# Optimization experiments

Hardware: AMD Instinct MI355X
Metric: run time of the kernel (lower is better)

The kernel has to match this reference:

```python
import jax, jax.numpy as jnp
import numpy as np

NEARZERO = 1e-5
NMUL = 16
NSTEP = 365
NGRID = 10000

# change_param_range: lb + raw * (ub - lb)
HBV_BOUNDS = {'parBETA': (1.0, 6.0), 'parK0': (0.05, 0.9), 'parBETAET': (0.3, 5.0)}
WL_BOUNDS = {'parFC': (50.0, 1000.0), 'parK1': (0.01, 0.5), 'parK2': (0.001, 0.2),
             'parLP': (0.2, 1.0), 'parPERC': (0.0, 10.0), 'parUZL': (0.0, 100.0),
             'parTT': (-2.5, 2.5), 'parCFMAX': (0.5, 10.0), 'parCFR': (0.0, 0.1),
             'parCWH': (0.0, 0.2), 'parC': (0.0, 1.0), 'parTRbound': (0.0, 20.0),
             'parAc': (0.0, 2500.0)}


def setup_inputs() -> dict:
    key = jax.random.key(0)
    kP, kT, kE, kp, kw, ka = jax.random.split(key, 6)
    P = jax.random.uniform(kP, (NSTEP, NGRID)) * 20.0          # precip [mm/day]
    T = jax.random.uniform(kT, (NSTEP, NGRID)) * 30.0 - 5.0    # temp [C]
    PET = jax.random.uniform(kE, (NSTEP, NGRID)) * 6.0         # PET [mm/day]
    x_hydro_model = jnp.stack([P, T, PET], axis=-1)            # [Nstep, Ngrid, 3]
    params_raw = jax.random.uniform(kp, (NSTEP, NGRID, 3, NMUL))
    waterloss_params_raw = jax.random.uniform(kw, (NGRID, 13, NMUL))
    ac_batch = jax.random.uniform(ka, (NGRID,)) * 3000.0       # drainage area proxy
    return {'x_hydro_model': x_hydro_model, 'params_raw': params_raw,
            'waterloss_params_raw': waterloss_params_raw, 'ac_batch': ac_batch}


def _scale_params(params_raw, waterloss_params_raw, static_idx=-1):
    p = {}
    for i, (name, (lb, ub)) in enumerate(HBV_BOUNDS.items()):
        p[name] = lb + params_raw[static_idx, :, i, :] * (ub - lb)       # [Ngrid, nmul]
    for i, (name, (lb, ub)) in enumerate(WL_BOUNDS.items()):
        p[name] = lb + waterloss_params_raw[:, i, :] * (ub - lb)         # [Ngrid, nmul]
    return p


def reference(x_hydro_model, params_raw, waterloss_params_raw, ac_batch):
    p = _scale_params(params_raw, waterloss_params_raw)
    P = x_hydro_model[:, :, 0]
    T = x_hydro_model[:, :, 1]
    PET = x_hydro_model[:, :, 2]

    acm = jnp.broadcast_to(ac_batch[:, None], (NGRID, NMUL))
    # regional flow is time-invariant (static params, static ac)
    rf = jnp.clip((acm - p['parAc']) / 1000.0, -1.0, 1.0)
    regional_flow = (rf * p['parTRbound'] * (acm < 2500.0).astype(rf.dtype)
                     + jnp.exp(jnp.clip(-(acm - 2500.0) / 50.0, -10.0, 0.0))
                       * p['parTRbound'] * (acm >= 2500.0).astype(rf.dtype))

    init_state = tuple(jnp.full((NGRID, NMUL), 0.001, dtype=jnp.float32) for _ in range(5))

    def step(carry, xs):
        SNOWPACK, MELTWATER, SM, SUZ, SLZ = carry
        Pt, Tt, PETt = xs
        Pm = Pt[:, None]
        Tm = Tt[:, None]
        PETm = PETt[:, None]
        warm = (Tm >= p['parTT']).astype(Pm.dtype)
        RAIN = Pm * warm
        SNOW = Pm * (1.0 - warm)
        SNOWPACK = SNOWPACK + SNOW
        melt = jnp.minimum(jnp.maximum(p['parCFMAX'] * (Tm - p['parTT']), 0.0), SNOWPACK)
        MELTWATER = MELTWATER + melt
        SNOWPACK = SNOWPACK - melt
        refreezing = jnp.minimum(
            jnp.maximum(p['parCFR'] * p['parCFMAX'] * (p['parTT'] - Tm), 0.0), MELTWATER)
        SNOWPACK = SNOWPACK + refreezing
        MELTWATER = MELTWATER - refreezing
        tosoil = jnp.maximum(MELTWATER - p['parCWH'] * SNOWPACK, 0.0)
        MELTWATER = MELTWATER - tosoil
        soil_wetness = jnp.clip((SM / p['parFC']) ** p['parBETA'], 0.0, 1.0)
        recharge = (RAIN + tosoil) * soil_wetness
        SM = SM + RAIN + tosoil - recharge
        excess = jnp.maximum(SM - p['parFC'], 0.0)
        SM = SM - excess
        evapfactor = jnp.clip((SM / (p['parLP'] * p['parFC'])) ** p['parBETAET'], 0.0, 1.0)
        ETact = jnp.minimum(SM, PETm * evapfactor)
        SM = jnp.maximum(SM - ETact, NEARZERO)
        capillary = jnp.minimum(SLZ, p['parC'] * SLZ * (1.0 - jnp.minimum(SM / p['parFC'], 1.0)))
        SM = jnp.maximum(SM + capillary, NEARZERO)
        SLZ = jnp.maximum(SLZ - capillary, NEARZERO)
        SUZ = SUZ + recharge + excess
        PERC = jnp.minimum(SUZ, p['parPERC'])
        SUZ = SUZ - PERC
        Q0 = p['parK0'] * jnp.maximum(SUZ - p['parUZL'], 0.0)
        SUZ = SUZ - Q0
        Q1 = p['parK1'] * SUZ
        SUZ = SUZ - Q1
        SLZ = SLZ + PERC
        SLZ = jnp.maximum(SLZ + regional_flow, 0.0)
        Q2 = p['parK2'] * SLZ
        SLZ = SLZ - Q2
        q = (Q0 + Q1 + Q2).mean(-1)  # Qsimavg over nmul components -> [Ngrid]
        return (SNOWPACK, MELTWATER, SM, SUZ, SLZ), q

    _, Qsimavg = jax.lax.scan(step, init_state, (P, T, PET))  # [Nstep, Ngrid]
    return Qsimavg
```

## Files before the change

### kernel.cpp

```cpp
#include <hip/hip_runtime.h>

#define NMUL 16
#define NSTEP 365
#define NGRID 10000
#define NEARZERO 1e-5f
#define UNROLL 4


__device__ __forceinline__ float fast_pow(float x, float y) {
    return __expf(y * __logf(x));
}

struct HbvP {
    float parBETA, parK0, parBETAET;
    float parFC, parK1, parK2, parLP, parPERC, parUZL, parTT,
          parCFMAX, parCWH, parC;
    float invFC, invLPFC, CFRCFMAX, regional_flow;
};

__device__ __forceinline__ float hbv_step(
    float Pm, float Tm, float PETm,
    float& SNOWPACK, float& MELTWATER, float& SM, float& SUZ, float& SLZ,
    const HbvP& p)
{
    const float RAIN = (Tm >= p.parTT) ? Pm : 0.0f;
    const float SNOW = Pm - RAIN;
    SNOWPACK += SNOW;
    const float melt = fminf(fmaxf(p.parCFMAX * (Tm - p.parTT), 0.0f), SNOWPACK);
    MELTWATER += melt;
    SNOWPACK  -= melt;
    const float refreezing = fminf(fmaxf(p.CFRCFMAX * (p.parTT - Tm), 0.0f), MELTWATER);
    SNOWPACK  += refreezing;
    MELTWATER -= refreezing;
    const float tosoil = fmaxf(MELTWATER - p.parCWH * SNOWPACK, 0.0f);
    MELTWATER -= tosoil;

    const float soil_wetness = fminf(fast_pow(SM * p.invFC, p.parBETA), 1.0f);
    const float recharge = (RAIN + tosoil) * soil_wetness;
    SM = SM + RAIN + tosoil - recharge;
    const float excess = fmaxf(SM - p.parFC, 0.0f);
    SM -= excess;
    const float evapfactor = fminf(fast_pow(SM * p.invLPFC, p.parBETAET), 1.0f);
    const float ETact = fminf(SM, PETm * evapfactor);
    SM = fmaxf(SM - ETact, NEARZERO);
    const float capillary = fminf(SLZ, p.parC * SLZ * (1.0f - fminf(SM * p.invFC, 1.0f)));
    SM  = fmaxf(SM + capillary, NEARZERO);
    SLZ = fmaxf(SLZ - capillary, NEARZERO);

    SUZ = SUZ + recharge + excess;
    const float PERCa = fminf(SUZ, p.parPERC);
    SUZ -= PERCa;
    const float Q0 = p.parK0 * fmaxf(SUZ - p.parUZL, 0.0f);
    SUZ -= Q0;
    const float Q1 = p.parK1 * SUZ;
    SUZ -= Q1;
    SLZ += PERCa;
    SLZ = fmaxf(SLZ + p.regional_flow, 0.0f);
    const float Q2 = p.parK2 * SLZ;
    SLZ -= Q2;

    return Q0 + Q1 + Q2;
}

__global__ __launch_bounds__(256) void hbv_kernel(
    const float* __restrict__ x,
    const float* __restrict__ pr,
    const float* __restrict__ wl,
    const float* __restrict__ ac,
    float* __restrict__ out)
{
    const int tid = blockIdx.x * blockDim.x + threadIdx.x;
    const int g = tid >> 4;
    const int m = tid & 15;

    HbvP p;
    const size_t pbase = ((size_t)(NSTEP - 1) * NGRID + (size_t)g) * 3 * NMUL + (size_t)m;
    p.parBETA   = 1.0f  + pr[pbase + 0 * NMUL] * 5.0f;
    p.parK0     = 0.05f + pr[pbase + 1 * NMUL] * 0.85f;
    p.parBETAET = 0.3f  + pr[pbase + 2 * NMUL] * 4.7f;

    const size_t wbase = (size_t)g * 13 * NMUL + (size_t)m;
    p.parFC    = 50.0f  + wl[wbase +  0 * NMUL] * 950.0f;
    p.parK1    = 0.01f  + wl[wbase +  1 * NMUL] * 0.49f;
    p.parK2    = 0.001f + wl[wbase +  2 * NMUL] * 0.199f;
    p.parLP    = 0.2f   + wl[wbase +  3 * NMUL] * 0.8f;
    p.parPERC  =          wl[wbase +  4 * NMUL] * 10.0f;
    p.parUZL   =          wl[wbase +  5 * NMUL] * 100.0f;
    p.parTT    = -2.5f  + wl[wbase +  6 * NMUL] * 5.0f;
    p.parCFMAX = 0.5f   + wl[wbase +  7 * NMUL] * 9.5f;
    const float parCFR =  wl[wbase +  8 * NMUL] * 0.1f;
    p.parCWH   =          wl[wbase +  9 * NMUL] * 0.2f;
    p.parC     =          wl[wbase + 10 * NMUL] * 1.0f;
    const float parTR  =  wl[wbase + 11 * NMUL] * 20.0f;
    const float parAc  =  wl[wbase + 12 * NMUL] * 2500.0f;

    const float acm = ac[g];
    if (acm < 2500.0f) {
        float rf = fminf(fmaxf((acm - parAc) * 0.001f, -1.0f), 1.0f);
        p.regional_flow = rf * parTR;
    } else {
        float e = fminf(fmaxf(-(acm - 2500.0f) * 0.02f, -10.0f), 0.0f);
        p.regional_flow = __expf(e) * parTR;
    }

    p.invFC    = 1.0f / p.parFC;
    p.invLPFC  = 1.0f / (p.parLP * p.parFC);
    p.CFRCFMAX = parCFR * p.parCFMAX;

    float SNOWPACK = 0.001f, MELTWATER = 0.001f, SM = 0.001f, SUZ = 0.001f, SLZ = 0.001f;

    float P0[UNROLL], T0[UNROLL], E0[UNROLL];
    #pragma unroll
    for (int u = 0; u < UNROLL; ++u) {
        const size_t xi = ((size_t)u * NGRID + (size_t)g) * 3;
        P0[u] = x[xi + 0]; T0[u] = x[xi + 1]; E0[u] = x[xi + 2];
    }

    int t = 0;
    for (int blk = 0; blk < 91; ++blk) {
        float P1[UNROLL], T1[UNROLL], E1[UNROLL];
        const int tn = t + UNROLL;
        if (blk < 90) {
            #pragma unroll
            for (int u = 0; u < UNROLL; ++u) {
                const size_t xi = ((size_t)(tn + u) * NGRID + (size_t)g) * 3;
                P1[u] = x[xi + 0]; T1[u] = x[xi + 1]; E1[u] = x[xi + 2];
            }
        } else {
            #pragma unroll
            for (int u = 0; u < UNROLL; ++u) { P1[u] = 0.f; T1[u] = 0.f; E1[u] = 0.f; }
        }

        float q[UNROLL];
        #pragma unroll
        for (int u = 0; u < UNROLL; ++u)
            q[u] = hbv_step(P0[u], T0[u], E0[u], SNOWPACK, MELTWATER, SM, SUZ, SLZ, p);

        #pragma unroll
        for (int s = 1; s < 16; s <<= 1) {
            #pragma unroll
            for (int u = 0; u < UNROLL; ++u)
                q[u] += __shfl_xor(q[u], s, 16);
        }
        if (m == 0) {
            #pragma unroll
            for (int u = 0; u < UNROLL; ++u)
                out[(size_t)(t + u) * NGRID + (size_t)g] = q[u] * 0.0625f;
        }

        #pragma unroll
        for (int u = 0; u < UNROLL; ++u) { P0[u] = P1[u]; T0[u] = T1[u]; E0[u] = E1[u]; }
        t = tn;
    }

    {
        const size_t xi = ((size_t)(NSTEP - 1) * NGRID + (size_t)g) * 3;
        float q = hbv_step(x[xi + 0], x[xi + 1], x[xi + 2],
                           SNOWPACK, MELTWATER, SM, SUZ, SLZ, p);
        #pragma unroll
        for (int s = 1; s < 16; s <<= 1) q += __shfl_xor(q, s, 16);
        if (m == 0) out[(size_t)(NSTEP - 1) * NGRID + (size_t)g] = q * 0.0625f;
    }
}

extern "C" void kernel_launch(void* const* d_in, const int* in_sizes, int n_in,
                              void* d_out, int out_size, void* d_ws, size_t ws_size,
                              hipStream_t stream) {
    const float* x  = (const float*)d_in[0];
    const float* pr = (const float*)d_in[1];
    const float* wl = (const float*)d_in[2];
    const float* ac = (const float*)d_in[3];
    float* out = (float*)d_out;

    const int total = NGRID * NMUL;
    const int block = 256;
    const int grid = (total + block - 1) / block;
    hbv_kernel<<<grid, block, 0, stream>>>(x, pr, wl, ac, out);
}
```

Before: 944.2 us.

## Replace shuffle reduction with DPP adds, unroll by 5, use 32-bit indexing

Replaces the ds-based shuffle reduction across 16 lanes with inline-asm DPP row_ror adds to cut cross-lane latency per step. Changes the unroll to 5 so 365 steps divide evenly and the tail step is removed. Also switches fast_pow to native exp2/log2 builtins, uses 32-bit offsets for addressing, and simplifies the refreeze term. The inline asm relies on manual hazard handling via s_nop, which the compiler cannot verify.

```diff
diff --git a/kernel.cpp b/kernel.cpp
--- a/kernel.cpp
+++ b/kernel.cpp
@@ -4,18 +4,22 @@
 #define NSTEP 365
 #define NGRID 10000
 #define NEARZERO 1e-5f
-#define UNROLL 4
+#define UNROLL 5
 
 
 __device__ __forceinline__ float fast_pow(float x, float y) {
+#if __has_builtin(__builtin_amdgcn_exp2f) && __has_builtin(__builtin_amdgcn_logf)
+    return __builtin_amdgcn_exp2f(y * __builtin_amdgcn_logf(x));
+#else
     return __expf(y * __logf(x));
+#endif
 }
 
 struct HbvP {
     float parBETA, parK0, parBETAET;
     float parFC, parK1, parK2, parLP, parPERC, parUZL, parTT,
-          parCFMAX, parCWH, parC;
-    float invFC, invLPFC, CFRCFMAX, regional_flow;
+          parCFMAX, parCWH, parC, parCFR;
+    float invFC, invLPFC, regional_flow;
 };
 
 __device__ __forceinline__ float hbv_step(
@@ -23,21 +27,24 @@
     float& SNOWPACK, float& MELTWATER, float& SM, float& SUZ, float& SLZ,
     const HbvP& p)
 {
-    const float RAIN = (Tm >= p.parTT) ? Pm : 0.0f;
+    const float d    = Tm - p.parTT;
+    const float RAIN = (d >= 0.0f) ? Pm : 0.0f;
     const float SNOW = Pm - RAIN;
     SNOWPACK += SNOW;
-    const float melt = fminf(fmaxf(p.parCFMAX * (Tm - p.parTT), 0.0f), SNOWPACK);
+    const float md   = p.parCFMAX * d;
+    const float melt = fminf(fmaxf(md, 0.0f), SNOWPACK);
     MELTWATER += melt;
     SNOWPACK  -= melt;
-    const float refreezing = fminf(fmaxf(p.CFRCFMAX * (p.parTT - Tm), 0.0f), MELTWATER);
+    const float refreezing = fminf(p.parCFR * fmaxf(-md, 0.0f), MELTWATER);
     SNOWPACK  += refreezing;
     MELTWATER -= refreezing;
     const float tosoil = fmaxf(MELTWATER - p.parCWH * SNOWPACK, 0.0f);
     MELTWATER -= tosoil;
 
     const float soil_wetness = fminf(fast_pow(SM * p.invFC, p.parBETA), 1.0f);
-    const float recharge = (RAIN + tosoil) * soil_wetness;
-    SM = SM + RAIN + tosoil - recharge;
+    const float rt = RAIN + tosoil;
+    const float recharge = rt * soil_wetness;
+    SM = SM + rt - recharge;
     const float excess = fmaxf(SM - p.parFC, 0.0f);
     SM -= excess;
     const float evapfactor = fminf(fast_pow(SM * p.invLPFC, p.parBETAET), 1.0f);
@@ -74,25 +81,25 @@
     const int m = tid & 15;
 
     HbvP p;
-    const size_t pbase = ((size_t)(NSTEP - 1) * NGRID + (size_t)g) * 3 * NMUL + (size_t)m;
-    p.parBETA   = 1.0f  + pr[pbase + 0 * NMUL] * 5.0f;
-    p.parK0     = 0.05f + pr[pbase + 1 * NMUL] * 0.85f;
-    p.parBETAET = 0.3f  + pr[pbase + 2 * NMUL] * 4.7f;
+    const unsigned pbase = ((unsigned)(NSTEP - 1) * NGRID + (unsigned)g) * (3u * NMUL) + (unsigned)m;
+    p.parBETA   = 1.0f  + pr[pbase + 0u * NMUL] * 5.0f;
+    p.parK0     = 0.05f + pr[pbase + 1u * NMUL] * 0.85f;
+    p.parBETAET = 0.3f  + pr[pbase + 2u * NMUL] * 4.7f;
 
-    const size_t wbase = (size_t)g * 13 * NMUL + (size_t)m;
-    p.parFC    = 50.0f  + wl[wbase +  0 * NMUL] * 950.0f;
-    p.parK1    = 0.01f  + wl[wbase +  1 * NMUL] * 0.49f;
-    p.parK2    = 0.001f + wl[wbase +  2 * NMUL] * 0.199f;
-    p.parLP    = 0.2f   + wl[wbase +  3 * NMUL] * 0.8f;
-    p.parPERC  =          wl[wbase +  4 * NMUL] * 10.0f;
-    p.parUZL   =          wl[wbase +  5 * NMUL] * 100.0f;
-    p.parTT    = -2.5f  + wl[wbase +  6 * NMUL] * 5.0f;
-    p.parCFMAX = 0.5f   + wl[wbase +  7 * NMUL] * 9.5f;
-    const float parCFR =  wl[wbase +  8 * NMUL] * 0.1f;
-    p.parCWH   =          wl[wbase +  9 * NMUL] * 0.2f;
-    p.parC     =          wl[wbase + 10 * NMUL] * 1.0f;
-    const float parTR  =  wl[wbase + 11 * NMUL] * 20.0f;
-    const float parAc  =  wl[wbase + 12 * NMUL] * 2500.0f;
+    const unsigned wbase = (unsigned)g * (13u * NMUL) + (unsigned)m;
+    p.parFC    = 50.0f  + wl[wbase +  0u * NMUL] * 950.0f;
+    p.parK1    = 0.01f  + wl[wbase +  1u * NMUL] * 0.49f;
+    p.parK2    = 0.001f + wl[wbase +  2u * NMUL] * 0.199f;
+    p.parLP    = 0.2f   + wl[wbase +  3u * NMUL] * 0.8f;
+    p.parPERC  =          wl[wbase +  4u * NMUL] * 10.0f;
+    p.parUZL   =          wl[wbase +  5u * NMUL] * 100.0f;
+    p.parTT    = -2.5f  + wl[wbase +  6u * NMUL] * 5.0f;
+    p.parCFMAX = 0.5f   + wl[wbase +  7u * NMUL] * 9.5f;
+    p.parCFR   =          wl[wbase +  8u * NMUL] * 0.1f;
+    p.parCWH   =          wl[wbase +  9u * NMUL] * 0.2f;
+    p.parC     =          wl[wbase + 10u * NMUL] * 1.0f;
+    const float parTR  =  wl[wbase + 11u * NMUL] * 20.0f;
+    const float parAc  =  wl[wbase + 12u * NMUL] * 2500.0f;
 
     const float acm = ac[g];
     if (acm < 2500.0f) {
@@ -103,63 +110,73 @@
         p.regional_flow = __expf(e) * parTR;
     }
 
-    p.invFC    = 1.0f / p.parFC;
-    p.invLPFC  = 1.0f / (p.parLP * p.parFC);
-    p.CFRCFMAX = parCFR * p.parCFMAX;
+    p.invFC   = 1.0f / p.parFC;
+    p.invLPFC = 1.0f / (p.parLP * p.parFC);
 
     float SNOWPACK = 0.001f, MELTWATER = 0.001f, SM = 0.001f, SUZ = 0.001f, SLZ = 0.001f;
+
+    unsigned xoff = (unsigned)g * 3u;
+    unsigned ooff = (unsigned)g;
 
     float P0[UNROLL], T0[UNROLL], E0[UNROLL];
     #pragma unroll
     for (int u = 0; u < UNROLL; ++u) {
-        const size_t xi = ((size_t)u * NGRID + (size_t)g) * 3;
-        P0[u] = x[xi + 0]; T0[u] = x[xi + 1]; E0[u] = x[xi + 2];
+        const unsigned xi = xoff + (unsigned)(u * NGRID * 3);
+        P0[u] = x[xi + 0u]; T0[u] = x[xi + 1u]; E0[u] = x[xi + 2u];
     }
+    xoff += (unsigned)(UNROLL * NGRID * 3);
 
-    int t = 0;
-    for (int blk = 0; blk < 91; ++blk) {
+    for (int blk = 0; blk < 73; ++blk) {
         float P1[UNROLL], T1[UNROLL], E1[UNROLL];
-        const int tn = t + UNROLL;
-        if (blk < 90) {
+        if (blk < 72) {
             #pragma unroll
             for (int u = 0; u < UNROLL; ++u) {
-                const size_t xi = ((size_t)(tn + u) * NGRID + (size_t)g) * 3;
-                P1[u] = x[xi + 0]; T1[u] = x[xi + 1]; E1[u] = x[xi + 2];
+                const unsigned xi = xoff + (unsigned)(u * NGRID * 3);
+                P1[u] = x[xi + 0u]; T1[u] = x[xi + 1u]; E1[u] = x[xi + 2u];
             }
         } else {
             #pragma unroll
             for (int u = 0; u < UNROLL; ++u) { P1[u] = 0.f; T1[u] = 0.f; E1[u] = 0.f; }
         }
+        xoff += (unsigned)(UNROLL * NGRID * 3);
 
         float q[UNROLL];
         #pragma unroll
         for (int u = 0; u < UNROLL; ++u)
             q[u] = hbv_step(P0[u], T0[u], E0[u], SNOWPACK, MELTWATER, SM, SUZ, SLZ, p);
 
-        #pragma unroll
-        for (int s = 1; s < 16; s <<= 1) {
-            #pragma unroll
-            for (int u = 0; u < UNROLL; ++u)
-                q[u] += __shfl_xor(q[u], s, 16);
-        }
+        asm("s_nop 3\n\t"
+            "v_add_f32 %0, %0, %0 row_ror:1 row_mask:0xf bank_mask:0xf\n\t"
+            "v_add_f32 %1, %1, %1 row_ror:1 row_mask:0xf bank_mask:0xf\n\t"
+            "v_add_f32 %2, %2, %2 row_ror:1 row_mask:0xf bank_mask:0xf\n\t"
+            "v_add_f32 %3, %3, %3 row_ror:1 row_mask:0xf bank_mask:0xf\n\t"
+            "v_add_f32 %4, %4, %4 row_ror:1 row_mask:0xf bank_mask:0xf\n\t"
+            "v_add_f32 %0, %0, %0 row_ror:2 row_mask:0xf bank_mask:0xf\n\t"
+            "v_add_f32 %1, %1, %1 row_ror:2 row_mask:0xf bank_mask:0xf\n\t"
+            "v_add_f32 %2, %2, %2 row_ror:2 row_mask:0xf bank_mask:0xf\n\t"
+            "v_add_f32 %3, %3, %3 row_ror:2 row_mask:0xf bank_mask:0xf\n\t"
+            "v_add_f32 %4, %4, %4 row_ror:2 row_mask:0xf bank_mask:0xf\n\t"
+            "v_add_f32 %0, %0, %0 row_ror:4 row_mask:0xf bank_mask:0xf\n\t"
+            "v_add_f32 %1, %1, %1 row_ror:4 row_mask:0xf bank_mask:0xf\n\t"
+            "v_add_f32 %2, %2, %2 row_ror:4 row_mask:0xf bank_mask:0xf\n\t"
+            "v_add_f32 %3, %3, %3 row_ror:4 row_mask:0xf bank_mask:0xf\n\t"
+            "v_add_f32 %4, %4, %4 row_ror:4 row_mask:0xf bank_mask:0xf\n\t"
+            "v_add_f32 %0, %0, %0 row_ror:8 row_mask:0xf bank_mask:0xf\n\t"
+            "v_add_f32 %1, %1, %1 row_ror:8 row_mask:0xf bank_mask:0xf\n\t"
+            "v_add_f32 %2, %2, %2 row_ror:8 row_mask:0xf bank_mask:0xf\n\t"
+            "v_add_f32 %3, %3, %3 row_ror:8 row_mask:0xf bank_mask:0xf\n\t"
+            "v_add_f32 %4, %4, %4 row_ror:8 row_mask:0xf bank_mask:0xf"
+            : "+v"(q[0]), "+v"(q[1]), "+v"(q[2]), "+v"(q[3]), "+v"(q[4]));
+
         if (m == 0) {
             #pragma unroll
             for (int u = 0; u < UNROLL; ++u)
-                out[(size_t)(t + u) * NGRID + (size_t)g] = q[u] * 0.0625f;
+                out[ooff + (unsigned)(u * NGRID)] = q[u] * 0.0625f;
         }
+        ooff += (unsigned)(UNROLL * NGRID);
 
         #pragma unroll
         for (int u = 0; u < UNROLL; ++u) { P0[u] = P1[u]; T0[u] = T1[u]; E0[u] = E1[u]; }
-        t = tn;
-    }
-
-    {
-        const size_t xi = ((size_t)(NSTEP - 1) * NGRID + (size_t)g) * 3;
-        float q = hbv_step(x[xi + 0], x[xi + 1], x[xi + 2],
-                           SNOWPACK, MELTWATER, SM, SUZ, SLZ, p);
-        #pragma unroll
-        for (int s = 1; s < 16; s <<= 1) q += __shfl_xor(q, s, 16);
-        if (m == 0) out[(size_t)(NSTEP - 1) * NGRID + (size_t)g] = q * 0.0625f;
     }
 }
 
```

Result: faster. 925.1 us (-2.0%).
